# Optimization experiments

Measured on AMD Instinct MI355X. Metric: run time of the kernel, lower is better.

The kernel has to match this reference:

```python
import jax, jax.numpy as jnp
import numpy as np

N, E = 50000, 800000
IN, HID, HEADS = 64, 32, 4


def setup_inputs() -> dict:
    key = jax.random.key(0)
    ks = jax.random.split(key, 18)
    x = jax.random.normal(ks[0], (N, IN), jnp.float32)
    edge_index = jax.random.randint(ks[1], (2, E), 0, N)

    def lin(k, fan_in, fan_out):
        kw, kb = jax.random.split(k)
        bound = 1.0 / np.sqrt(fan_in)
        W = jax.random.uniform(kw, (fan_in, fan_out), jnp.float32, -bound, bound)
        b = jax.random.uniform(kb, (fan_out,), jnp.float32, -bound, bound)
        return W, b

    # layer 1: in=IN, out=HID per head, heads=HEADS, concat=True -> out dim HID*HEADS
    Wq1, bq1 = lin(ks[2], IN, HEADS * HID)
    Wk1, bk1 = lin(ks[3], IN, HEADS * HID)
    Wv1, bv1 = lin(ks[4], IN, HEADS * HID)
    Ws1, bs1 = lin(ks[5], IN, HEADS * HID)  # root/skip lin
    # layer 2: in=HID*HEADS, out=HID, heads=1, concat=False
    IN2 = HID * HEADS
    Wq2, bq2 = lin(ks[6], IN2, HID)
    Wk2, bk2 = lin(ks[7], IN2, HID)
    Wv2, bv2 = lin(ks[8], IN2, HID)
    Ws2, bs2 = lin(ks[9], IN2, HID)
    return dict(x=x, edge_index=edge_index,
                Wq1=Wq1, bq1=bq1, Wk1=Wk1, bk1=bk1, Wv1=Wv1, bv1=bv1, Ws1=Ws1, bs1=bs1,
                Wq2=Wq2, bq2=bq2, Wk2=Wk2, bk2=bk2, Wv2=Wv2, bv2=bv2, Ws2=Ws2, bs2=bs2)


def transformer_conv(x, src, dst, Wq, bq, Wk, bk, Wv, bv, Ws, bs, heads, out_ch, concat):
    """PyG TransformerConv (eval mode, root_weight=True, beta=False)."""
    n = x.shape[0]
    q = (x @ Wq + bq).reshape(n, heads, out_ch)  # [N,H,C]
    k = (x @ Wk + bk).reshape(n, heads, out_ch)
    v = (x @ Wv + bv).reshape(n, heads, out_ch)
    # per-edge attention logits: q_i . k_j / sqrt(C)
    logits = jnp.einsum('ehc,ehc->eh', q[dst], k[src]) / jnp.sqrt(jnp.float32(out_ch))
    # segment softmax over incoming edges of each target node
    m = jax.ops.segment_max(logits, dst, num_segments=n)          # [N,H]
    p = jnp.exp(logits - m[dst])                                   # [E,H]
    denom = jax.ops.segment_sum(p, dst, num_segments=n)            # [N,H]
    alpha = p / denom[dst]                                         # [E,H]
    agg = jax.ops.segment_sum(alpha[:, :, None] * v[src], dst, num_segments=n)  # [N,H,C]
    if concat:
        o = agg.reshape(n, heads * out_ch)
    else:
        o = agg.mean(axis=1)
    return o + x @ Ws + bs


def reference(x, edge_index,
              Wq1, bq1, Wk1, bk1, Wv1, bv1, Ws1, bs1,
              Wq2, bq2, Wk2, bk2, Wv2, bv2, Ws2, bs2):
    src, dst = edge_index[0], edge_index[1]
    h = transformer_conv(x, src, dst, Wq1, bq1, Wk1, bk1, Wv1, bv1, Ws1, bs1,
                         HEADS, HID, True)
    h = jax.nn.elu(h)
    out = transformer_conv(h, src, dst, Wq2, bq2, Wk2, bk2, Wv2, bv2, Ws2, bs2,
                           1, HID, False)
    return out
```

## Files before the change

### kernel.cpp

```cpp
#include <hip/hip_runtime.h>
#include <hip/hip_bf16.h>
#include <hip/hip_fp8.h>

#define N_NODES 50000
#define N_EDGES 800000
#define HB 3125
#define GB1 1563
#define NBS 49

static constexpr float SCALE = 0.17677669529663687f;

typedef __attribute__((ext_vector_type(8))) short bf16x8;
typedef __attribute__((ext_vector_type(4))) float f32x4;
typedef __attribute__((ext_vector_type(2))) float f32x2;
#define MFMA16 __builtin_amdgcn_mfma_f32_16x16x32_bf16

static __device__ inline unsigned short f2bf(float f) {
    __hip_bfloat16 h = __float2bfloat16(f);
    return __builtin_bit_cast(unsigned short, h);
}
static __device__ inline unsigned char f2fp8(float f) {
    __hip_fp8_e4m3 h(f);
    return __builtin_bit_cast(unsigned char, h);
}
static __device__ inline float2 bfpair(unsigned u) {
    return make_float2(__uint_as_float(u << 16),
                       __uint_as_float(u & 0xffff0000u));
}
static __device__ inline float dot8f8(const float* q, uint2 u) {
    f32x2 a = __builtin_amdgcn_cvt_pk_f32_fp8(u.x, false);
    f32x2 b = __builtin_amdgcn_cvt_pk_f32_fp8(u.x, true);
    f32x2 c = __builtin_amdgcn_cvt_pk_f32_fp8(u.y, false);
    f32x2 d = __builtin_amdgcn_cvt_pk_f32_fp8(u.y, true);
    return q[0]*a[0] + q[1]*a[1] + q[2]*b[0] + q[3]*b[1]
         + q[4]*c[0] + q[5]*c[1] + q[6]*d[0] + q[7]*d[1];
}
static __device__ inline float dot8(const float* q, uint4 u) {
    float2 a = bfpair(u.x), b = bfpair(u.y), c = bfpair(u.z), d = bfpair(u.w);
    return q[0]*a.x + q[1]*a.y + q[2]*b.x + q[3]*b.y
         + q[4]*c.x + q[5]*c.y + q[6]*d.x + q[7]*d.y;
}
static __device__ inline void acc8(float* acc, float w, uint4 u) {
    float2 a = bfpair(u.x), b = bfpair(u.y), c = bfpair(u.z), d = bfpair(u.w);
    acc[0] += w*a.x; acc[1] += w*a.y; acc[2] += w*b.x; acc[3] += w*b.y;
    acc[4] += w*c.x; acc[5] += w*c.y; acc[6] += w*d.x; acc[7] += w*d.y;
}
static __device__ inline void unpack8(float* o, uint4 u) {
    float2 a = bfpair(u.x), b = bfpair(u.y), c = bfpair(u.z), d = bfpair(u.w);
    o[0]=a.x; o[1]=a.y; o[2]=b.x; o[3]=b.y; o[4]=c.x; o[5]=c.y; o[6]=d.x; o[7]=d.y;
}
static __device__ inline bf16x8 cvt8(const float* p) {
    float4 f0 = *(const float4*)p;
    float4 f1 = *(const float4*)(p + 4);
    bf16x8 r;
    r[0] = (short)f2bf(f0.x); r[1] = (short)f2bf(f0.y);
    r[2] = (short)f2bf(f0.z); r[3] = (short)f2bf(f0.w);
    r[4] = (short)f2bf(f1.x); r[5] = (short)f2bf(f1.y);
    r[6] = (short)f2bf(f1.z); r[7] = (short)f2bf(f1.w);
    return r;
}


__global__ __launch_bounds__(256) void k_prep(
    const float* __restrict__ Wq1, const float* __restrict__ Wk1,
    const float* __restrict__ Wv1, const float* __restrict__ Ws1,
    const float* __restrict__ Wq2, const float* __restrict__ Wk2,
    const float* __restrict__ Wv2, const float* __restrict__ Ws2,
    unsigned short* __restrict__ Wf1, unsigned short* __restrict__ Wf2)
{
    int id = blockIdx.x * 256 + threadIdx.x;
    if (id < 32768) {
        int j = id & 7, l = (id >> 3) & 63, ks = (id >> 9) & 1, nt = (id >> 10) & 7, m = (id >> 13) & 3;
        const float* W = (m == 0) ? Wq1 : (m == 1) ? Wk1 : (m == 2) ? Wv1 : Ws1;
        int k = ks * 32 + ((l >> 4) << 3) + j;
        int c = nt * 16 + (l & 15);
        Wf1[id] = f2bf(W[k * 128 + c]);
    } else if (id < 49152) {
        int id2 = id - 32768;
        int j = id2 & 7, l = (id2 >> 3) & 63, ks = (id2 >> 9) & 3, g = (id2 >> 11) & 7;
        int m = g >> 1, t = g & 1;
        const float* W = (m == 0) ? Wq2 : (m == 1) ? Wk2 : (m == 2) ? Wv2 : Ws2;
        int k = ks * 32 + ((l >> 4) << 3) + j;
        int c = t * 16 + (l & 15);
        Wf2[id2] = f2bf(W[k * 32 + c]);
    }
}


__global__ __launch_bounds__(256) void k_big(
    const int* __restrict__ dst, int* __restrict__ cnt, int* __restrict__ rank,
    const float* __restrict__ x, const unsigned short* __restrict__ Wf1,
    const float* __restrict__ bq, const float* __restrict__ bk,
    const float* __restrict__ bv, const float* __restrict__ bs,
    unsigned short* __restrict__ qs1, unsigned char* __restrict__ k8,
    unsigned short* __restrict__ v1, int n)
{
    __shared__ unsigned char smem[4 * 8704];
    if (blockIdx.x >= GB1) {
        int e = (blockIdx.x - GB1) * 256 + threadIdx.x;
        rank[e] = atomicAdd(&cnt[dst[e]], 1);
        return;
    }
    int w = threadIdx.x >> 6;
    int l = threadIdx.x & 63;
    int rb = blockIdx.x * 32;
    int lr = l & 15, lk = l >> 4;
    f32x4 acc[2][8];
#pragma unroll
    for (int mt = 0; mt < 2; ++mt)
#pragma unroll
        for (int nt = 0; nt < 8; ++nt) acc[mt][nt] = (f32x4){0.f, 0.f, 0.f, 0.f};
#pragma unroll
    for (int ks = 0; ks < 2; ++ks) {
        bf16x8 a[2];
#pragma unroll
        for (int mt = 0; mt < 2; ++mt) {
            int r = rb + mt * 16 + lr;
            if (r >= n) r = n - 1;
            a[mt] = cvt8(x + (size_t)r * 64 + ks * 32 + lk * 8);
        }
#pragma unroll
        for (int nt = 0; nt < 8; ++nt) {
            bf16x8 b = *(const bf16x8*)(Wf1 + (size_t)((w * 8 + nt) * 1024 + ks * 512 + l * 8));
            acc[0][nt] = MFMA16(a[0], b, acc[0][nt], 0, 0, 0);
            acc[1][nt] = MFMA16(a[1], b, acc[1][nt], 0, 0, 0);
        }
    }
    const float* bptr = (w == 0) ? bq : (w == 1) ? bk : (w == 2) ? bv : bs;
    unsigned char* my = smem + w * 8704;
    if (w == 1) {
        unsigned char* lb = my;
#pragma unroll
        for (int nt = 0; nt < 8; ++nt) {
            float bias = bptr[nt * 16 + lr];
#pragma unroll
            for (int mt = 0; mt < 2; ++mt)
#pragma unroll
                for (int i = 0; i < 4; ++i)
                    lb[(mt * 16 + lk * 4 + i) * 144 + nt * 16 + lr] = f2fp8(acc[mt][nt][i] + bias);
        }
#pragma unroll
        for (int p = 0; p < 8; ++p) {
            int rl = p * 4 + lk;
            int r = rb + rl;
            if (r < n) {
                uint2 val = *(const uint2*)(lb + rl * 144 + lr * 8);
                *(uint2*)(k8 + (size_t)r * 128 + lr * 8) = val;
            }
        }
    } else {
        unsigned short* ls = (unsigned short*)my;
#pragma unroll
        for (int nt = 0; nt < 8; ++nt) {
            float bias = bptr[nt * 16 + lr];
#pragma unroll
            for (int mt = 0; mt < 2; ++mt)
#pragma unroll
                for (int i = 0; i < 4; ++i)
                    ls[(mt * 16 + lk * 4 + i) * 136 + nt * 16 + lr] = f2bf(acc[mt][nt][i] + bias);
        }
        unsigned short* outp = (w == 0) ? qs1 : (w == 3) ? qs1 + 128 : v1;
        size_t stride = (w == 2) ? 128 : 256;
#pragma unroll
        for (int p = 0; p < 8; ++p) {
            int rl = p * 4 + lk;
            int r = rb + rl;
            if (r < n) {
                uint4 val = *(const uint4*)(ls + rl * 136 + lr * 8);
                *(uint4*)(outp + (size_t)r * stride + lr * 8) = val;
            }
        }
    }
}


__global__ __launch_bounds__(256) void k_scan(const int* __restrict__ cnt,
                                              int* __restrict__ row,
                                              int* __restrict__ bsum,
                                              int* __restrict__ boff,
                                              int* __restrict__ ctr, int n) {
    __shared__ int wsum[4];
    __shared__ int lastBlk;
    int t = threadIdx.x;
    int base = blockIdx.x * 1024 + t * 4;
    int v0 = (base + 0 < n) ? cnt[base + 0] : 0;
    int v1 = (base + 1 < n) ? cnt[base + 1] : 0;
    int v2 = (base + 2 < n) ? cnt[base + 2] : 0;
    int v3 = (base + 3 < n) ? cnt[base + 3] : 0;
    int s = v0 + v1 + v2 + v3;
    int lane = t & 63, wid = t >> 6;
    int sc = s;
#pragma unroll
    for (int d = 1; d < 64; d <<= 1) {
        int o = __shfl_up(sc, d);
        if (lane >= d) sc += o;
    }
    if (lane == 63) wsum[wid] = sc;
    __syncthreads();
    int woff = 0;
    for (int w = 0; w < wid; ++w) woff += wsum[w];
    int excl = woff + sc - s;
    if (base + 0 < n) row[base + 0] = excl;
    if (base + 1 < n) row[base + 1] = excl + v0;
    if (base + 2 < n) row[base + 2] = excl + v0 + v1;
    if (base + 3 < n) row[base + 3] = excl + v0 + v1 + v2;
    if (t == 255) {
        bsum[blockIdx.x] = woff + sc;
        __threadfence();
        lastBlk = (atomicAdd(ctr, 1) == (int)gridDim.x - 1);
    }
    __syncthreads();
    if (lastBlk && t < 64) {
        __threadfence();
        int v = (t < NBS) ? ((volatile int*)bsum)[t] : 0;
        int sc2 = v;
#pragma unroll
        for (int d = 1; d < 64; d <<= 1) {
            int o = __shfl_up(sc2, d);
            if (t >= d) sc2 += o;
        }
        boff[t] = sc2 - v;
        if (t == (N_NODES >> 10)) row[N_NODES] = N_EDGES - (sc2 - v);
    }
}


__global__ void k_scat(const int* __restrict__ src, const int* __restrict__ dst,
                       const int* __restrict__ row, const int* __restrict__ boff,
                       const int* __restrict__ rank, int* __restrict__ col) {
    int e = blockIdx.x * 256 + threadIdx.x;
    int de = dst[e];
    col[row[de] + boff[de >> 10] + rank[e]] = src[e];
}


__global__ __launch_bounds__(256) void k_gemm2m(
    const unsigned short* __restrict__ h1b, const unsigned short* __restrict__ Wf2,
    const float* __restrict__ bq, const float* __restrict__ bk,
    const float* __restrict__ bv, const float* __restrict__ bs,
    unsigned short* __restrict__ qs2, unsigned short* __restrict__ kv2, int n)
{
    __shared__ unsigned short lds[4][32][72];
    int w = threadIdx.x >> 6;
    int l = threadIdx.x & 63;
    int half = w & 1;
    int rb = blockIdx.x * 64 + (w >> 1) * 32;
    int lr = l & 15, lk = l >> 4;
    f32x4 acc[2][4];
#pragma unroll
    for (int mt = 0; mt < 2; ++mt)
#pragma unroll
        for (int nt = 0; nt < 4; ++nt) acc[mt][nt] = (f32x4){0.f, 0.f, 0.f, 0.f};
#pragma unroll
    for (int ks = 0; ks < 4; ++ks) {
        bf16x8 a[2];
#pragma unroll
        for (int mt = 0; mt < 2; ++mt) {
            int r = rb + mt * 16 + lr;
            if (r >= n) r = n - 1;
            a[mt] = *(const bf16x8*)(h1b + (size_t)r * 128 + ks * 32 + lk * 8);
        }
#pragma unroll
        for (int nt = 0; nt < 4; ++nt) {
            int g = half * 4 + nt;
            bf16x8 b = *(const bf16x8*)(Wf2 + (size_t)((g * 4 + ks) * 512 + l * 8));
            acc[0][nt] = MFMA16(a[0], b, acc[0][nt], 0, 0, 0);
            acc[1][nt] = MFMA16(a[1], b, acc[1][nt], 0, 0, 0);
        }
    }
#pragma unroll
    for (int nt = 0; nt < 4; ++nt) {
        int g = half * 4 + nt;
        int mat = g >> 1;
        int c = (g * 16 + lr) & 31;
        const float* bp = (mat == 0) ? bq : (mat == 1) ? bk : (mat == 2) ? bv : bs;
        float bias = bp[c];
#pragma unroll
        for (int mt = 0; mt < 2; ++mt)
#pragma unroll
            for (int i = 0; i < 4; ++i)
                lds[w][mt * 16 + lk * 4 + i][nt * 16 + lr] = f2bf(acc[mt][nt][i] + bias);
    }
    unsigned short* outA = (half == 0) ? qs2 : kv2 + 32;
    unsigned short* outB = (half == 0) ? kv2 : qs2 + 32;
    int rl8 = l >> 3, ci = (l & 7) * 4;
#pragma unroll
    for (int p = 0; p < 4; ++p) {
        int rl = p * 8 + rl8;
        int r = rb + rl;
        if (r < n) {
            uint2 va = *(const uint2*)&lds[w][rl][ci];
            *(uint2*)(outA + (size_t)r * 64 + ci) = va;
            uint2 vb = *(const uint2*)&lds[w][rl][32 + ci];
            *(uint2*)(outB + (size_t)r * 64 + ci) = vb;
        }
    }
}


__global__ __launch_bounds__(256) void k_agg1(
    const unsigned short* __restrict__ qs1, const unsigned char* __restrict__ k8,
    const unsigned short* __restrict__ v1,
    const int* __restrict__ row, const int* __restrict__ boff,
    const int* __restrict__ col, uint4* __restrict__ h1b, int n)
{
    int i = blockIdx.x * 4 + (threadIdx.x >> 6);
    if (i >= n) return;
    int lane = threadIdx.x & 63;
    int slot = lane >> 4, w = lane & 15;
    float q[8];
    unpack8(q, *(const uint4*)(qs1 + (size_t)i * 256 + w * 8));
    float acc[8] = {};
    float d = 0.f;
    int s = row[i] + boff[i >> 10];
    int e = row[i + 1] + boff[(i + 1) >> 10];
    for (int t = s; t < e; t += 8) {
        int ta = t + slot, tb = t + 4 + slot;
        bool va = ta < e, vb = tb < e;
        int ja = col[va ? ta : s];
        int jb = col[vb ? tb : s];
        uint2 ka = *(const uint2*)(k8 + (size_t)ja * 128 + w * 8);
        uint2 kb = *(const uint2*)(k8 + (size_t)jb * 128 + w * 8);
        uint4 vA = *(const uint4*)(v1 + (size_t)ja * 128 + w * 8);
        uint4 vB = *(const uint4*)(v1 + (size_t)jb * 128 + w * 8);
        float la = dot8f8(q, ka);
        float lb = dot8f8(q, kb);
        la += __shfl_xor(la, 1);  lb += __shfl_xor(lb, 1);
        la += __shfl_xor(la, 2);  lb += __shfl_xor(lb, 2);
        float wa = va ? __expf(la * SCALE) : 0.f;
        float wb = vb ? __expf(lb * SCALE) : 0.f;
        d += wa + wb;
        acc8(acc, wa, vA);
        acc8(acc, wb, vB);
    }
#pragma unroll
    for (int m = 16; m <= 32; m <<= 1) {
        d += __shfl_xor(d, m);
#pragma unroll
        for (int c = 0; c < 8; ++c) acc[c] += __shfl_xor(acc[c], m);
    }
    if (slot == 0) {
        float inv = (d > 0.f) ? 1.f / d : 0.f;
        float sv[8];
        unpack8(sv, *(const uint4*)(qs1 + (size_t)i * 256 + 128 + w * 8));
        unsigned o[4];
#pragma unroll
        for (int p = 0; p < 4; ++p) {
            float rx = acc[2 * p] * inv + sv[2 * p];
            float ry = acc[2 * p + 1] * inv + sv[2 * p + 1];
            rx = (rx > 0.f) ? rx : expm1f(rx);
            ry = (ry > 0.f) ? ry : expm1f(ry);
            o[p] = ((unsigned)f2bf(ry) << 16) | (unsigned)f2bf(rx);
        }
        h1b[(size_t)i * 16 + w] = make_uint4(o[0], o[1], o[2], o[3]);
    }
}


__global__ __launch_bounds__(256) void k_agg2(
    const unsigned short* __restrict__ qs2, const unsigned short* __restrict__ kv2,
    const int* __restrict__ row, const int* __restrict__ boff,
    const int* __restrict__ col, float* __restrict__ out, int n)
{
    int i = blockIdx.x * 4 + (threadIdx.x >> 6);
    if (i >= n) return;
    int lane = threadIdx.x & 63;
    int slot = lane >> 2, qr = lane & 3;
    float q[8];
    unpack8(q, *(const uint4*)(qs2 + (size_t)i * 64 + qr * 8));
    float acc[8] = {};
    float d = 0.f;
    int s = row[i] + boff[i >> 10];
    int e = row[i + 1] + boff[(i + 1) >> 10];
    for (int t = s; t < e; t += 16) {
        int te = t + slot;
        bool va = te < e;
        int j = col[va ? te : s];
        const unsigned short* p = kv2 + (size_t)j * 64;
        uint4 ku = *(const uint4*)(p + qr * 8);
        uint4 vu = *(const uint4*)(p + 32 + qr * 8);
        float lg = dot8(q, ku);
        lg += __shfl_xor(lg, 1);
        lg += __shfl_xor(lg, 2);
        float wv = va ? __expf(lg * SCALE) : 0.f;
        d += wv;
        acc8(acc, wv, vu);
    }
#pragma unroll
    for (int m = 4; m <= 32; m <<= 1) {
        d += __shfl_xor(d, m);
#pragma unroll
        for (int c = 0; c < 8; ++c) acc[c] += __shfl_xor(acc[c], m);
    }
    if (slot == 0) {
        float inv = (d > 0.f) ? 1.f / d : 0.f;
        float sv[8];
        unpack8(sv, *(const uint4*)(qs2 + (size_t)i * 64 + 32 + qr * 8));
        float4 o0, o1;
        o0.x = acc[0] * inv + sv[0];
        o0.y = acc[1] * inv + sv[1];
        o0.z = acc[2] * inv + sv[2];
        o0.w = acc[3] * inv + sv[3];
        o1.x = acc[4] * inv + sv[4];
        o1.y = acc[5] * inv + sv[5];
        o1.z = acc[6] * inv + sv[6];
        o1.w = acc[7] * inv + sv[7];
        *(float4*)&out[(size_t)i * 32 + qr * 8] = o0;
        *(float4*)&out[(size_t)i * 32 + qr * 8 + 4] = o1;
    }
}


extern "C" void kernel_launch(void* const* d_in, const int* in_sizes, int n_in,
                              void* d_out, int out_size, void* d_ws, size_t ws_size,
                              hipStream_t stream)
{
    const int N = N_NODES, E = N_EDGES;
    const float* x   = (const float*)d_in[0];
    const int* edge  = (const int*)d_in[1];
    const int* src   = edge;
    const int* dst   = edge + E;
    const float* Wq1 = (const float*)d_in[2];  const float* bq1 = (const float*)d_in[3];
    const float* Wk1 = (const float*)d_in[4];  const float* bk1 = (const float*)d_in[5];
    const float* Wv1 = (const float*)d_in[6];  const float* bv1 = (const float*)d_in[7];
    const float* Ws1 = (const float*)d_in[8];  const float* bs1 = (const float*)d_in[9];
    const float* Wq2 = (const float*)d_in[10]; const float* bq2 = (const float*)d_in[11];
    const float* Wk2 = (const float*)d_in[12]; const float* bk2 = (const float*)d_in[13];
    const float* Wv2 = (const float*)d_in[14]; const float* bv2 = (const float*)d_in[15];
    const float* Ws2 = (const float*)d_in[16]; const float* bs2 = (const float*)d_in[17];

    char* ws = (char*)d_ws;
    size_t off = 0;
    auto alloc = [&](size_t bytes) -> void* {
        void* p = ws + off;
        off += (bytes + 255) & ~(size_t)255;
        return p;
    };
    unsigned short* qs1 = (unsigned short*)alloc((size_t)N * 256 * 2);
    unsigned char*  k8  = (unsigned char*)alloc((size_t)N * 128);
    unsigned short* v1  = (unsigned short*)alloc((size_t)N * 128 * 2);
    unsigned short* h1b = (unsigned short*)alloc((size_t)N * 128 * 2);
    unsigned short* qs2 = (unsigned short*)alloc((size_t)N * 64 * 2);
    unsigned short* kv2 = (unsigned short*)alloc((size_t)N * 64 * 2);
    unsigned short* Wf1 = (unsigned short*)alloc(32768 * 2);
    unsigned short* Wf2 = (unsigned short*)alloc(16384 * 2);
    int* row_ptr  = (int*)alloc((size_t)(N + 1) * 4);
    int* cnt      = (int*)alloc((size_t)(N + 64) * 4);
    int* ctr      = cnt + N;
    int* rank     = (int*)alloc((size_t)E * 4);
    int* colb     = (int*)alloc((size_t)E * 4);
    int* bsum     = (int*)alloc(64 * 4);
    int* boff     = (int*)alloc(64 * 4);

    hipMemsetAsync(cnt, 0, (size_t)(N + 64) * 4, stream);
    k_prep<<<192, 256, 0, stream>>>(Wq1, Wk1, Wv1, Ws1, Wq2, Wk2, Wv2, Ws2, Wf1, Wf2);
    k_big<<<GB1 + HB, 256, 0, stream>>>(dst, cnt, rank,
                                        x, Wf1, bq1, bk1, bv1, bs1, qs1, k8, v1, N);
    k_scan<<<NBS, 256, 0, stream>>>(cnt, row_ptr, bsum, boff, ctr, N);
    k_scat<<<HB, 256, 0, stream>>>(src, dst, row_ptr, boff, rank, colb);
    k_agg1<<<(N + 3) / 4, 256, 0, stream>>>(qs1, k8, v1, row_ptr, boff, colb, (uint4*)h1b, N);
    k_gemm2m<<<(N + 63) / 64, 256, 0, stream>>>(h1b, Wf2, bq2, bk2, bv2, bs2, qs2, kv2, N);
    k_agg2<<<(N + 3) / 4, 256, 0, stream>>>(qs2, kv2, row_ptr, boff, colb, (float*)d_out, N);
}
```

Baseline: 162.7 us.

## Regroup kernels: fuse degree counting with weight prep, scan with layer-1 GEMM

Moves the per-edge degree atomic counting into the weight-prep kernel and the CSR prefix scan into the layer-1 projection GEMM kernel as extra blocks, dropping one kernel launch and rebalancing the work between them. The GEMM epilogue now stages one 16-row tile at a time, which halves its shared-memory buffer and may raise occupancy. The fusion relies on the scan's last-block detection now comparing against NBS instead of the grid size.

```diff
diff --git a/kernel.cpp b/kernel.cpp
--- a/kernel.cpp
+++ b/kernel.cpp
@@ -61,14 +61,20 @@
 }
 
 
-__global__ __launch_bounds__(256) void k_prep(
+__global__ __launch_bounds__(256) void k_ph(
+    const int* __restrict__ dst, int* __restrict__ cnt, int* __restrict__ rank,
     const float* __restrict__ Wq1, const float* __restrict__ Wk1,
     const float* __restrict__ Wv1, const float* __restrict__ Ws1,
     const float* __restrict__ Wq2, const float* __restrict__ Wk2,
     const float* __restrict__ Wv2, const float* __restrict__ Ws2,
     unsigned short* __restrict__ Wf1, unsigned short* __restrict__ Wf2)
 {
-    int id = blockIdx.x * 256 + threadIdx.x;
+    if (blockIdx.x < HB) {
+        int e = blockIdx.x * 256 + threadIdx.x;
+        rank[e] = atomicAdd(&cnt[dst[e]], 1);
+        return;
+    }
+    int id = (blockIdx.x - HB) * 256 + threadIdx.x;
     if (id < 32768) {
         int j = id & 7, l = (id >> 3) & 63, ks = (id >> 9) & 1, nt = (id >> 10) & 7, m = (id >> 13) & 3;
         const float* W = (m == 0) ? Wq1 : (m == 1) ? Wk1 : (m == 2) ? Wv1 : Ws1;
@@ -87,18 +93,61 @@
 }
 
 
-__global__ __launch_bounds__(256) void k_big(
-    const int* __restrict__ dst, int* __restrict__ cnt, int* __restrict__ rank,
+__global__ __launch_bounds__(256) void k_gs(
+    const int* __restrict__ cnt, int* __restrict__ row, int* __restrict__ bsum,
+    int* __restrict__ boff, int* __restrict__ ctr,
     const float* __restrict__ x, const unsigned short* __restrict__ Wf1,
     const float* __restrict__ bq, const float* __restrict__ bk,
     const float* __restrict__ bv, const float* __restrict__ bs,
     unsigned short* __restrict__ qs1, unsigned char* __restrict__ k8,
     unsigned short* __restrict__ v1, int n)
 {
-    __shared__ unsigned char smem[4 * 8704];
+    __shared__ unsigned char smem[4 * 4352];
     if (blockIdx.x >= GB1) {
-        int e = (blockIdx.x - GB1) * 256 + threadIdx.x;
-        rank[e] = atomicAdd(&cnt[dst[e]], 1);
+        __shared__ int wsum[4];
+        __shared__ int lastBlk;
+        int b = blockIdx.x - GB1;
+        int t = threadIdx.x;
+        int base = b * 1024 + t * 4;
+        int v0 = (base + 0 < n) ? cnt[base + 0] : 0;
+        int v1i = (base + 1 < n) ? cnt[base + 1] : 0;
+        int v2 = (base + 2 < n) ? cnt[base + 2] : 0;
+        int v3 = (base + 3 < n) ? cnt[base + 3] : 0;
+        int s = v0 + v1i + v2 + v3;
+        int lane = t & 63, wid = t >> 6;
+        int sc = s;
+#pragma unroll
+        for (int d = 1; d < 64; d <<= 1) {
+            int o = __shfl_up(sc, d);
+            if (lane >= d) sc += o;
+        }
+        if (lane == 63) wsum[wid] = sc;
+        __syncthreads();
+        int woff = 0;
+        for (int w = 0; w < wid; ++w) woff += wsum[w];
+        int excl = woff + sc - s;
+        if (base + 0 < n) row[base + 0] = excl;
+        if (base + 1 < n) row[base + 1] = excl + v0;
+        if (base + 2 < n) row[base + 2] = excl + v0 + v1i;
+        if (base + 3 < n) row[base + 3] = excl + v0 + v1i + v2;
+        if (t == 255) {
+            bsum[b] = woff + sc;
+            __threadfence();
+            lastBlk = (atomicAdd(ctr, 1) == NBS - 1);
+        }
+        __syncthreads();
+        if (lastBlk && t < 64) {
+            __threadfence();
+            int v = (t < NBS) ? ((volatile int*)bsum)[t] : 0;
+            int sc2 = v;
+#pragma unroll
+            for (int d = 1; d < 64; d <<= 1) {
+                int o = __shfl_up(sc2, d);
+                if (t >= d) sc2 += o;
+            }
+            boff[t] = sc2 - v;
+            if (t == (N_NODES >> 10)) row[N_NODES] = N_EDGES - (sc2 - v);
+        }
         return;
     }
     int w = threadIdx.x >> 6;
@@ -127,100 +176,48 @@
         }
     }
     const float* bptr = (w == 0) ? bq : (w == 1) ? bk : (w == 2) ? bv : bs;
-    unsigned char* my = smem + w * 8704;
-    if (w == 1) {
-        unsigned char* lb = my;
-#pragma unroll
-        for (int nt = 0; nt < 8; ++nt) {
-            float bias = bptr[nt * 16 + lr];
-#pragma unroll
-            for (int mt = 0; mt < 2; ++mt)
+    unsigned char* my = smem + w * 4352;
+#pragma unroll
+    for (int mt = 0; mt < 2; ++mt) {
+        if (w == 1) {
+            unsigned char* lb = my;
+#pragma unroll
+            for (int nt = 0; nt < 8; ++nt) {
+                float bias = bptr[nt * 16 + lr];
 #pragma unroll
                 for (int i = 0; i < 4; ++i)
-                    lb[(mt * 16 + lk * 4 + i) * 144 + nt * 16 + lr] = f2fp8(acc[mt][nt][i] + bias);
-        }
-#pragma unroll
-        for (int p = 0; p < 8; ++p) {
-            int rl = p * 4 + lk;
-            int r = rb + rl;
-            if (r < n) {
-                uint2 val = *(const uint2*)(lb + rl * 144 + lr * 8);
-                *(uint2*)(k8 + (size_t)r * 128 + lr * 8) = val;
+                    lb[(lk * 4 + i) * 144 + nt * 16 + lr] = f2fp8(acc[mt][nt][i] + bias);
             }
-        }
-    } else {
-        unsigned short* ls = (unsigned short*)my;
-#pragma unroll
-        for (int nt = 0; nt < 8; ++nt) {
-            float bias = bptr[nt * 16 + lr];
-#pragma unroll
-            for (int mt = 0; mt < 2; ++mt)
+#pragma unroll
+            for (int p = 0; p < 4; ++p) {
+                int rl = p * 4 + lk;
+                int r = rb + mt * 16 + rl;
+                if (r < n) {
+                    uint2 val = *(const uint2*)(lb + rl * 144 + lr * 8);
+                    *(uint2*)(k8 + (size_t)r * 128 + lr * 8) = val;
+                }
+            }
+        } else {
+            unsigned short* ls = (unsigned short*)my;
+#pragma unroll
+            for (int nt = 0; nt < 8; ++nt) {
+                float bias = bptr[nt * 16 + lr];
 #pragma unroll
                 for (int i = 0; i < 4; ++i)
-                    ls[(mt * 16 + lk * 4 + i) * 136 + nt * 16 + lr] = f2bf(acc[mt][nt][i] + bias);
-        }
-        unsigned short* outp = (w == 0) ? qs1 : (w == 3) ? qs1 + 128 : v1;
-        size_t stride = (w == 2) ? 128 : 256;
-#pragma unroll
-        for (int p = 0; p < 8; ++p) {
-            int rl = p * 4 + lk;
-            int r = rb + rl;
-            if (r < n) {
-                uint4 val = *(const uint4*)(ls + rl * 136 + lr * 8);
-                *(uint4*)(outp + (size_t)r * stride + lr * 8) = val;
+                    ls[(lk * 4 + i) * 136 + nt * 16 + lr] = f2bf(acc[mt][nt][i] + bias);
             }
-        }
-    }
-}
-
-
-__global__ __launch_bounds__(256) void k_scan(const int* __restrict__ cnt,
-                                              int* __restrict__ row,
-                                              int* __restrict__ bsum,
-                                              int* __restrict__ boff,
-                                              int* __restrict__ ctr, int n) {
-    __shared__ int wsum[4];
-    __shared__ int lastBlk;
-    int t = threadIdx.x;
-    int base = blockIdx.x * 1024 + t * 4;
-    int v0 = (base + 0 < n) ? cnt[base + 0] : 0;
-    int v1 = (base + 1 < n) ? cnt[base + 1] : 0;
-    int v2 = (base + 2 < n) ? cnt[base + 2] : 0;
-    int v3 = (base + 3 < n) ? cnt[base + 3] : 0;
-    int s = v0 + v1 + v2 + v3;
-    int lane = t & 63, wid = t >> 6;
-    int sc = s;
-#pragma unroll
-    for (int d = 1; d < 64; d <<= 1) {
-        int o = __shfl_up(sc, d);
-        if (lane >= d) sc += o;
-    }
-    if (lane == 63) wsum[wid] = sc;
-    __syncthreads();
-    int woff = 0;
-    for (int w = 0; w < wid; ++w) woff += wsum[w];
-    int excl = woff + sc - s;
-    if (base + 0 < n) row[base + 0] = excl;
-    if (base + 1 < n) row[base + 1] = excl + v0;
-    if (base + 2 < n) row[base + 2] = excl + v0 + v1;
-    if (base + 3 < n) row[base + 3] = excl + v0 + v1 + v2;
-    if (t == 255) {
-        bsum[blockIdx.x] = woff + sc;
-        __threadfence();
-        lastBlk = (atomicAdd(ctr, 1) == (int)gridDim.x - 1);
-    }
-    __syncthreads();
-    if (lastBlk && t < 64) {
-        __threadfence();
-        int v = (t < NBS) ? ((volatile int*)bsum)[t] : 0;
-        int sc2 = v;
-#pragma unroll
-        for (int d = 1; d < 64; d <<= 1) {
-            int o = __shfl_up(sc2, d);
-            if (t >= d) sc2 += o;
-        }
-        boff[t] = sc2 - v;
-        if (t == (N_NODES >> 10)) row[N_NODES] = N_EDGES - (sc2 - v);
+            unsigned short* outp = (w == 0) ? qs1 : (w == 3) ? qs1 + 128 : v1;
+            size_t stride = (w == 2) ? 128 : 256;
+#pragma unroll
+            for (int p = 0; p < 4; ++p) {
+                int rl = p * 4 + lk;
+                int r = rb + mt * 16 + rl;
+                if (r < n) {
+                    uint4 val = *(const uint4*)(ls + rl * 136 + lr * 8);
+                    *(uint4*)(outp + (size_t)r * stride + lr * 8) = val;
+                }
+            }
+        }
     }
 }
 
@@ -453,10 +450,11 @@
     int* boff     = (int*)alloc(64 * 4);
 
     hipMemsetAsync(cnt, 0, (size_t)(N + 64) * 4, stream);
-    k_prep<<<192, 256, 0, stream>>>(Wq1, Wk1, Wv1, Ws1, Wq2, Wk2, Wv2, Ws2, Wf1, Wf2);
-    k_big<<<GB1 + HB, 256, 0, stream>>>(dst, cnt, rank,
+    k_ph<<<HB + 192, 256, 0, stream>>>(dst, cnt, rank,
+                                       Wq1, Wk1, Wv1, Ws1, Wq2, Wk2, Wv2, Ws2,
+                                       Wf1, Wf2);
+    k_gs<<<GB1 + NBS, 256, 0, stream>>>(cnt, row_ptr, bsum, boff, ctr,
                                         x, Wf1, bq1, bk1, bv1, bs1, qs1, k8, v1, N);
-    k_scan<<<NBS, 256, 0, stream>>>(cnt, row_ptr, bsum, boff, ctr, N);
     k_scat<<<HB, 256, 0, stream>>>(src, dst, row_ptr, boff, rank, colb);
     k_agg1<<<(N + 3) / 4, 256, 0, stream>>>(qs1, k8, v1, row_ptr, boff, colb, (uint4*)h1b, N);
     k_gemm2m<<<(N + 63) / 64, 256, 0, stream>>>(h1b, Wf2, bq2, bk2, bv2, bs2, qs2, kv2, N);
```

Measured after the change: 168.1 us. 3.3% more time.
